# Kernel optimization log

Hardware: AMD Instinct MI355X
Metric: run time of the kernel (lower is better)

The kernel has to match this reference:

```python
import jax, jax.numpy as jnp
import numpy as np
from jax import lax

H, W, C = 24, 8, 128
HW = H * W
PART = 4
SA_K = 49  # CBAM spatial-attention kernel size (default of CBAMBlock)
EPS = 1e-5


def conv2d(x, w, b, pad_h, pad_w):
    y = lax.conv_general_dilated(x, w, (1, 1), [(pad_h, pad_h), (pad_w, pad_w)],
                                 dimension_numbers=('NCHW', 'OIHW', 'NCHW'))
    return y + b[None, :, None, None]


def cbam(x, se_w1, se_w2, sa_w, sa_b):
    # Channel attention: shared MLP on global max- and avg-pooled descriptors.
    mx = x.max(axis=(2, 3))          # [n, c]
    av = x.mean(axis=(2, 3))         # [n, c]
    def se(v):
        return jax.nn.relu(v @ se_w1.T) @ se_w2.T
    ca = jax.nn.sigmoid(se(mx) + se(av))[:, :, None, None]
    out = x * ca
    # Spatial attention: 49x49 conv on [max, mean] over channels.
    smx = out.max(axis=1, keepdims=True)
    sav = out.mean(axis=1, keepdims=True)
    s = jnp.concatenate([smx, sav], axis=1)      # [n, 2, H, W]
    sa = jax.nn.sigmoid(conv2d(s, sa_w, sa_b, SA_K // 2, SA_K // 2))
    return out * sa + x


def position_aware_max(score6, dim):
    # score6: [p, g, hr, wr, hs, ws]; fixed-length (part_rows) row window,
    # start clamped to [0, h - part_rows] -> vectorized sliding-window max.
    part_rows = H // PART
    half = part_rows // 2
    starts = jnp.clip(jnp.arange(H) - half, 0, H - part_rows)
    if dim == 0:
        m = score6.max(axis=3)            # max over wr -> [p, g, hr, hs, ws]
        mi = jnp.moveaxis(m, 3, 0)        # [hs, p, g, hr, ws]
        def f(m_i, st):
            return lax.dynamic_slice_in_dim(m_i, st, part_rows, axis=2).max(axis=2)
        out = jax.vmap(f)(mi, starts)     # [h, p, g, ws]
    else:
        m = score6.max(axis=5)            # max over ws -> [p, g, hr, wr, hs]
        mi = jnp.moveaxis(m, 2, 0)        # [hr, p, g, wr, hs]
        def f(m_i, st):
            return lax.dynamic_slice_in_dim(m_i, st, part_rows, axis=3).max(axis=3)
        out = jax.vmap(f)(mi, starts)     # [h, p, g, wr]
    p, g = score6.shape[0], score6.shape[1]
    return jnp.moveaxis(out, 0, 2).reshape(p, g, HW)


def bn_eval(x, gamma, beta, mean, var):
    return (x - mean) * (gamma / jnp.sqrt(var + EPS)) + beta


def setup_inputs() -> dict:
    key = jax.random.key(0)
    ks = jax.random.split(key, 8)
    red = 16
    return {
        'prob_fea': jax.random.normal(ks[0], (32, C, H, W), jnp.float32),
        'gal_fea': jax.random.normal(ks[1], (32, C, H, W), jnp.float32),
        'se_w1': jax.random.normal(ks[2], (C // red, C), jnp.float32) * 0.05,
        'se_w2': jax.random.normal(ks[3], (C, C // red), jnp.float32) * 0.05,
        'sa_w': jax.random.normal(ks[4], (1, 2, SA_K, SA_K), jnp.float32) * 0.02,
        'sa_b': jnp.zeros((1,), jnp.float32),
        'bn_g': jnp.ones((1,), jnp.float32),
        'bn_b': jnp.zeros((1,), jnp.float32),
        'bn_m': jnp.zeros((1,), jnp.float32),
        'bn_v': jnp.ones((1,), jnp.float32),
        'fc_w': jnp.full((1, HW), 1.0 / HW, jnp.float32),
        'fc_b': jax.random.normal(ks[5], (1,), jnp.float32) * 0.01,
        'lbn_g': jnp.ones((1,), jnp.float32),
        'lbn_b': jnp.zeros((1,), jnp.float32),
        'lbn_m': jnp.zeros((1,), jnp.float32),
        'lbn_v': jnp.ones((1,), jnp.float32),
    }


def reference(prob_fea, gal_fea, se_w1, se_w2, sa_w, sa_b,
              bn_g, bn_b, bn_m, bn_v, fc_w, fc_b,
              lbn_g, lbn_b, lbn_m, lbn_v):
    pf = cbam(prob_fea, se_w1, se_w2, sa_w, sa_b)
    gf = cbam(gal_fea, se_w1, se_w2, sa_w, sa_b)
    p, g = pf.shape[0], gf.shape[0]
    pf = pf.reshape(p, C, HW)
    gf = gf.reshape(g, C, HW)
    # pairwise feature matching: [p, g, r(gal spatial), s(prob spatial)]
    score = jnp.einsum('pcs,gcr->pgrs', pf, gf)
    score6 = score.reshape(p, g, H, W, H, W)
    s1 = position_aware_max(score6, 0)  # [p, g, HW]
    s2 = position_aware_max(score6, 1)  # [p, g, HW]
    sc = jnp.concatenate([s1, s2], axis=-1).reshape(-1, HW)  # [p*g*2, HW]
    sc = bn_eval(sc, bn_g, bn_b, bn_m, bn_v)
    y = sc @ fc_w.T + fc_b                  # [p*g*2, 1]
    y = y.reshape(-1, 2).sum(axis=1, keepdims=True)
    y = bn_eval(y, lbn_g, lbn_b, lbn_m, lbn_v)
    return jax.nn.sigmoid(y).reshape(p, g)
```

## Files before the change

kernel.cpp:

```cpp
#include <hip/hip_runtime.h>
#include <hip/hip_bf16.h>

#define HH 24
#define WW 8
#define HWSZ 192
#define CC 128
#define EPSV 1e-5f

#define M1LD 200
#define M2LD 28

typedef __attribute__((ext_vector_type(8))) short bf16x8;
typedef __attribute__((ext_vector_type(4))) float f32x4;

__device__ __forceinline__ float sigmoidf_(float x) { return 1.0f / (1.0f + expf(-x)); }

__device__ __forceinline__ unsigned short f2bf(float f) {
    unsigned int u = __float_as_uint(f);
    unsigned int r = (u + 0x7fffu + ((u >> 16) & 1u)) >> 16;
    return (unsigned short)r;
}
__device__ __forceinline__ float bf2f(unsigned short s) {
    return __uint_as_float((unsigned int)s << 16);
}

__global__ __launch_bounds__(512) void cbam_stats(
    const float* __restrict__ prob, const float* __restrict__ gal,
    const float* __restrict__ se_w1, const float* __restrict__ se_w2,
    const float* __restrict__ sa_w, const float* __restrict__ sa_b,
    float* __restrict__ ca_out, float* __restrict__ sa_out)
{
    __shared__ float mxs[CC], avs[CC], hid[16], cas[CC];
    __shared__ float smx2[2 * HWSZ], sav2[2 * HWSZ];
    __shared__ float wbuf[2 * 49 * 49];

    int n = blockIdx.x;
    const float* x = (n < 32) ? prob + (size_t)n * CC * HWSZ : gal + (size_t)(n - 32) * CC * HWSZ;

    int tid = threadIdx.x, l = tid & 63, w = tid >> 6;

    for (int i = tid; i < 2 * 49 * 49; i += 512) wbuf[i] = sa_w[i];

    for (int i = 0; i < 16; ++i) {
        int c = w * 16 + i;
        const float* row = x + c * HWSZ;
        float a = row[l], b = row[l + 64], d = row[l + 128];
        float mv = fmaxf(a, fmaxf(b, d));
        float sv = a + b + d;
        #pragma unroll
        for (int m = 1; m < 64; m <<= 1) {
            mv = fmaxf(mv, __shfl_xor(mv, m));
            sv += __shfl_xor(sv, m);
        }
        if (l == 0) { mxs[c] = mv; avs[c] = sv * (1.0f / HWSZ); }
    }
    __syncthreads();

    if (tid < 256) {
        int j = tid >> 4, chunk = tid & 15;
        const float* v = (j < 8) ? mxs : avs;
        const float* wrow = se_w1 + (j & 7) * CC + chunk * 8;
        const float* vv = v + chunk * 8;
        float acc = 0.f;
        #pragma unroll
        for (int k = 0; k < 8; ++k) acc += vv[k] * wrow[k];
        #pragma unroll
        for (int m = 1; m < 16; m <<= 1) acc += __shfl_xor(acc, m);
        if (chunk == 0) hid[j] = fmaxf(acc, 0.f);
    }
    __syncthreads();

    if (tid < CC) {
        float acc = 0.f;
        #pragma unroll
        for (int j = 0; j < 8; ++j) acc += (hid[j] + hid[8 + j]) * se_w2[tid * 8 + j];
        cas[tid] = sigmoidf_(acc);
        ca_out[n * CC + tid] = cas[tid];
    }
    __syncthreads();

    if (tid < 2 * HWSZ) {
        int s = tid >> 1, half = tid & 1;
        int c0 = half * 64;
        float mv = -INFINITY, sv = 0.f;
        #pragma unroll 4
        for (int k = 0; k < 64; ++k) {
            float v = x[(c0 + k) * HWSZ + s] * cas[c0 + k];
            mv = fmaxf(mv, v); sv += v;
        }
        smx2[half * HWSZ + s] = mv; sav2[half * HWSZ + s] = sv;
    }
    __syncthreads();

    if (tid < HWSZ) {
        int y = tid >> 3, xx = tid & 7;
        float acc = sa_b[0];
        for (int iy = 0; iy < HH; ++iy) {
            int wy = iy - y + 24;
            const float* w0 = wbuf + wy * 49;
            const float* w1 = wbuf + 2401 + wy * 49;
            #pragma unroll
            for (int ix = 0; ix < WW; ++ix) {
                int wx = ix - xx + 24;
                int sp = iy * 8 + ix;
                float s0 = fmaxf(smx2[sp], smx2[HWSZ + sp]);
                float s1 = (sav2[sp] + sav2[HWSZ + sp]) * (1.0f / CC);
                acc += s0 * w0[wx] + s1 * w1[wx];
            }
        }
        sa_out[n * HWSZ + tid] = sigmoidf_(acc);
    }
}

__global__ __launch_bounds__(256) void cbam_apply(
    const float* __restrict__ prob, const float* __restrict__ gal,
    const float* __restrict__ ca_buf, const float* __restrict__ sa_buf,
    __hip_bfloat16* __restrict__ pf_t, __hip_bfloat16* __restrict__ gf_t)
{
    __shared__ unsigned short T[16][136];
    __shared__ float sash[16];

    int n = blockIdx.x / 12;
    int s0 = (blockIdx.x % 12) * 16;
    const float* x = (n < 32) ? prob + (size_t)n * CC * HWSZ : gal + (size_t)(n - 32) * CC * HWSZ;
    __hip_bfloat16* dst = (n < 32) ? pf_t + (size_t)n * HWSZ * CC : gf_t + (size_t)(n - 32) * HWSZ * CC;

    int tid = threadIdx.x;
    if (tid < 16) sash[tid] = sa_buf[n * HWSZ + s0 + tid];
    __syncthreads();

    int c = tid >> 1, half = tid & 1;
    float ca = ca_buf[n * CC + c];
    const float* xp = x + c * HWSZ + s0 + half * 8;
    float4 va = *(const float4*)xp;
    float4 vb = *(const float4*)(xp + 4);
    int r0 = half * 8;
    T[r0 + 0][c] = f2bf(va.x * (1.f + ca * sash[r0 + 0]));
    T[r0 + 1][c] = f2bf(va.y * (1.f + ca * sash[r0 + 1]));
    T[r0 + 2][c] = f2bf(va.z * (1.f + ca * sash[r0 + 2]));
    T[r0 + 3][c] = f2bf(va.w * (1.f + ca * sash[r0 + 3]));
    T[r0 + 4][c] = f2bf(vb.x * (1.f + ca * sash[r0 + 4]));
    T[r0 + 5][c] = f2bf(vb.y * (1.f + ca * sash[r0 + 5]));
    T[r0 + 6][c] = f2bf(vb.z * (1.f + ca * sash[r0 + 6]));
    T[r0 + 7][c] = f2bf(vb.w * (1.f + ca * sash[r0 + 7]));
    __syncthreads();

    int s_l = tid >> 4, c8 = (tid & 15) * 8;
    const unsigned int* src = (const unsigned int*)&T[s_l][c8];
    unsigned int* d32 = (unsigned int*)(dst + (s0 + s_l) * CC + c8);
    d32[0] = src[0]; d32[1] = src[1]; d32[2] = src[2]; d32[3] = src[3];
}

__global__ __launch_bounds__(384) void score_kernel(
    const __hip_bfloat16* __restrict__ pf_t, const __hip_bfloat16* __restrict__ gf_t,
    const float* __restrict__ bn_g, const float* __restrict__ bn_b,
    const float* __restrict__ bn_m, const float* __restrict__ bn_v,
    const float* __restrict__ fc_w, const float* __restrict__ fc_b,
    const float* __restrict__ lbn_g, const float* __restrict__ lbn_b,
    const float* __restrict__ lbn_m, const float* __restrict__ lbn_v,
    float* __restrict__ out)
{
    __shared__ __align__(16) char bstage[2][4096];
    __shared__ unsigned short M1b[24 * M1LD];
    __shared__ unsigned short M2b[HWSZ * M2LD];
    __shared__ float red[6], wred[6];

    int bi = blockIdx.x;
    int p = bi >> 5, g = bi & 31;
    int tid = threadIdx.x, l = tid & 63, w = tid >> 6;

    const __hip_bfloat16* A = gf_t + (size_t)g * HWSZ * CC;
    const __hip_bfloat16* B = pf_t + (size_t)p * HWSZ * CC;

    int row_a = l & 15;
    int koff = (l >> 4) * 8;

    #define STAGE_B(bufidx, st_)                                                         \
        if (w < 4) {                                                                     \
            const __hip_bfloat16* src = B + ((st_) * 16 + (l & 15)) * CC                 \
                                          + (w * 4 + (l >> 4)) * 8;                      \
            __builtin_amdgcn_global_load_lds(                                            \
                (const __attribute__((address_space(1))) void*)src,                      \
                (__attribute__((address_space(3))) void*)(&bstage[bufidx][w * 1024]),    \
                16, 0, 0);                                                               \
        }

    STAGE_B(0, 0)

    bf16x8 afr[2][4];
    #pragma unroll
    for (int rt = 0; rt < 2; ++rt) {
        const __hip_bfloat16* ap = A + (w * 32 + rt * 16 + row_a) * CC + koff;
        #pragma unroll
        for (int ks = 0; ks < 4; ++ks)
            afr[rt][ks] = *(const bf16x8*)(ap + ks * 32);
    }
    __syncthreads();

    for (int st = 0; st < 12; ++st) {
        int cur = st & 1;
        if (st < 11) { STAGE_B(cur ^ 1, st + 1) }

        const char* bb = bstage[cur];
        bf16x8 b0 = *(const bf16x8*)(bb + 0 * 1024 + l * 16);
        bf16x8 b1 = *(const bf16x8*)(bb + 1 * 1024 + l * 16);
        bf16x8 b2 = *(const bf16x8*)(bb + 2 * 1024 + l * 16);
        bf16x8 b3 = *(const bf16x8*)(bb + 3 * 1024 + l * 16);

        #pragma unroll
        for (int rt = 0; rt < 2; ++rt) {
            f32x4 acc = {0.f, 0.f, 0.f, 0.f};
            acc = __builtin_amdgcn_mfma_f32_16x16x32_bf16(afr[rt][0], b0, acc, 0, 0, 0);
            acc = __builtin_amdgcn_mfma_f32_16x16x32_bf16(afr[rt][1], b1, acc, 0, 0, 0);
            acc = __builtin_amdgcn_mfma_f32_16x16x32_bf16(afr[rt][2], b2, acc, 0, 0, 0);
            acc = __builtin_amdgcn_mfma_f32_16x16x32_bf16(afr[rt][3], b3, acc, 0, 0, 0);

            int RT = w * 2 + rt;

            float mrow = fmaxf(fmaxf(acc[0], acc[1]), fmaxf(acc[2], acc[3]));
            mrow = fmaxf(mrow, __shfl_xor(mrow, 16));
            if (((l >> 4) & 1) == 0)
                M1b[(2 * RT + (l >> 5)) * M1LD + st * 16 + (l & 15)] = f2bf(mrow);

            float v0 = acc[0], v1 = acc[1], v2 = acc[2], v3 = acc[3];
            #pragma unroll
            for (int m = 1; m < 8; m <<= 1) {
                v0 = fmaxf(v0, __shfl_xor(v0, m));
                v1 = fmaxf(v1, __shfl_xor(v1, m));
                v2 = fmaxf(v2, __shfl_xor(v2, m));
                v3 = fmaxf(v3, __shfl_xor(v3, m));
            }
            if ((l & 7) == 0) {
                int hs = st * 2 + ((l >> 3) & 1);
                int rbase = RT * 16 + (l >> 4) * 4;
                M2b[(rbase + 0) * M2LD + hs] = f2bf(v0);
                M2b[(rbase + 1) * M2LD + hs] = f2bf(v1);
                M2b[(rbase + 2) * M2LD + hs] = f2bf(v2);
                M2b[(rbase + 3) * M2LD + hs] = f2bf(v3);
            }
        }
        __syncthreads();
    }

    float part = 0.f, wpart = 0.f;
    if (tid < HWSZ) {
        int h = tid >> 3;
        int st0 = h - 3; if (st0 < 0) st0 = 0; if (st0 > 18) st0 = 18;
        float v1 = -INFINITY, v2 = -INFINITY;
        #pragma unroll
        for (int i = 0; i < 6; ++i) {
            v1 = fmaxf(v1, bf2f(M1b[(st0 + i) * M1LD + tid]));
            v2 = fmaxf(v2, bf2f(M2b[tid * M2LD + st0 + i]));
        }
        float fw = fc_w[tid];
        part = fw * (v1 + v2);
        wpart = fw;
    }
    #pragma unroll
    for (int m = 1; m < 64; m <<= 1) {
        part  += __shfl_xor(part, m);
        wpart += __shfl_xor(wpart, m);
    }
    if (l == 0) { red[w] = part; wred[w] = wpart; }
    __syncthreads();

    if (tid == 0) {
        float total = red[0] + red[1] + red[2] + red[3] + red[4] + red[5];
        float Wsum  = wred[0] + wred[1] + wred[2] + wred[3] + wred[4] + wred[5];
        float k1 = bn_g[0] * rsqrtf(bn_v[0] + EPSV);
        float Y = k1 * total + 2.f * ((bn_b[0] - k1 * bn_m[0]) * Wsum + fc_b[0]);
        float kl = lbn_g[0] * rsqrtf(lbn_v[0] + EPSV);
        float Z = (Y - lbn_m[0]) * kl + lbn_b[0];
        out[bi] = 1.f / (1.f + expf(-Z));
    }
}

extern "C" void kernel_launch(void* const* d_in, const int* in_sizes, int n_in,
                              void* d_out, int out_size, void* d_ws, size_t ws_size,
                              hipStream_t stream)
{
    const float* prob  = (const float*)d_in[0];
    const float* gal   = (const float*)d_in[1];
    const float* se_w1 = (const float*)d_in[2];
    const float* se_w2 = (const float*)d_in[3];
    const float* sa_w  = (const float*)d_in[4];
    const float* sa_b  = (const float*)d_in[5];
    const float* bn_g  = (const float*)d_in[6];
    const float* bn_b  = (const float*)d_in[7];
    const float* bn_m  = (const float*)d_in[8];
    const float* bn_v  = (const float*)d_in[9];
    const float* fc_w  = (const float*)d_in[10];
    const float* fc_b  = (const float*)d_in[11];
    const float* lbn_g = (const float*)d_in[12];
    const float* lbn_b = (const float*)d_in[13];
    const float* lbn_m = (const float*)d_in[14];
    const float* lbn_v = (const float*)d_in[15];

    __hip_bfloat16* pf_t = (__hip_bfloat16*)d_ws;
    __hip_bfloat16* gf_t = pf_t + (size_t)32 * HWSZ * CC;
    float* ca_buf = (float*)(gf_t + (size_t)32 * HWSZ * CC);
    float* sa_buf = ca_buf + 64 * CC;
    float* out = (float*)d_out;

    cbam_stats<<<64, 512, 0, stream>>>(prob, gal, se_w1, se_w2, sa_w, sa_b, ca_buf, sa_buf);
    cbam_apply<<<768, 256, 0, stream>>>(prob, gal, ca_buf, sa_buf, pf_t, gf_t);
    score_kernel<<<1024, 384, 0, stream>>>(pf_t, gf_t, bn_g, bn_b, bn_m, bn_v,
                                           fc_w, fc_b, lbn_g, lbn_b, lbn_m, lbn_v, out);
}
```

Measured before the change: 154.0 us.

## Preload all B tiles to LDS and compute transposed MFMA for column max

Loads the whole 192x128 probe tile into LDS up front instead of double-buffering one stage at a time, which removes the per-stage barrier inside the score loop. It also issues a second, operand-swapped MFMA chain so the column-direction max can be taken with a single xor-shuffle instead of a three-step shuffle butterfly over four values. This doubles MFMA work and raises LDS use to about 48KB per block for staging alone, which may lower occupancy.

```diff
diff --git a/kernel.cpp b/kernel.cpp
--- a/kernel.cpp
+++ b/kernel.cpp
@@ -160,7 +160,7 @@
     const float* __restrict__ lbn_m, const float* __restrict__ lbn_v,
     float* __restrict__ out)
 {
-    __shared__ __align__(16) char bstage[2][4096];
+    __shared__ __align__(16) char Bs[12 * 4096];
     __shared__ unsigned short M1b[24 * M1LD];
     __shared__ unsigned short M2b[HWSZ * M2LD];
     __shared__ float red[6], wred[6];
@@ -172,21 +172,19 @@
     const __hip_bfloat16* A = gf_t + (size_t)g * HWSZ * CC;
     const __hip_bfloat16* B = pf_t + (size_t)p * HWSZ * CC;
 
+    #pragma unroll
+    for (int i = 0; i < 8; ++i) {
+        int idx = w * 8 + i;
+        const __hip_bfloat16* src = B + ((idx >> 2) * 16 + (l & 15)) * CC
+                                      + ((idx & 3) * 4 + (l >> 4)) * 8;
+        __builtin_amdgcn_global_load_lds(
+            (const __attribute__((address_space(1))) void*)src,
+            (__attribute__((address_space(3))) void*)(&Bs[idx * 1024]),
+            16, 0, 0);
+    }
+
     int row_a = l & 15;
     int koff = (l >> 4) * 8;
-
-    #define STAGE_B(bufidx, st_)                                                         \
-        if (w < 4) {                                                                     \
-            const __hip_bfloat16* src = B + ((st_) * 16 + (l & 15)) * CC                 \
-                                          + (w * 4 + (l >> 4)) * 8;                      \
-            __builtin_amdgcn_global_load_lds(                                            \
-                (const __attribute__((address_space(1))) void*)src,                      \
-                (__attribute__((address_space(3))) void*)(&bstage[bufidx][w * 1024]),    \
-                16, 0, 0);                                                               \
-        }
-
-    STAGE_B(0, 0)
-
     bf16x8 afr[2][4];
     #pragma unroll
     for (int rt = 0; rt < 2; ++rt) {
@@ -198,10 +196,7 @@
     __syncthreads();
 
     for (int st = 0; st < 12; ++st) {
-        int cur = st & 1;
-        if (st < 11) { STAGE_B(cur ^ 1, st + 1) }
-
-        const char* bb = bstage[cur];
+        const char* bb = Bs + st * 4096;
         bf16x8 b0 = *(const bf16x8*)(bb + 0 * 1024 + l * 16);
         bf16x8 b1 = *(const bf16x8*)(bb + 1 * 1024 + l * 16);
         bf16x8 b2 = *(const bf16x8*)(bb + 2 * 1024 + l * 16);
@@ -209,38 +204,31 @@
 
         #pragma unroll
         for (int rt = 0; rt < 2; ++rt) {
-            f32x4 acc = {0.f, 0.f, 0.f, 0.f};
-            acc = __builtin_amdgcn_mfma_f32_16x16x32_bf16(afr[rt][0], b0, acc, 0, 0, 0);
-            acc = __builtin_amdgcn_mfma_f32_16x16x32_bf16(afr[rt][1], b1, acc, 0, 0, 0);
-            acc = __builtin_amdgcn_mfma_f32_16x16x32_bf16(afr[rt][2], b2, acc, 0, 0, 0);
-            acc = __builtin_amdgcn_mfma_f32_16x16x32_bf16(afr[rt][3], b3, acc, 0, 0, 0);
+            f32x4 acc1 = {0.f, 0.f, 0.f, 0.f};
+            f32x4 acc2 = {0.f, 0.f, 0.f, 0.f};
+            acc1 = __builtin_amdgcn_mfma_f32_16x16x32_bf16(afr[rt][0], b0, acc1, 0, 0, 0);
+            acc2 = __builtin_amdgcn_mfma_f32_16x16x32_bf16(b0, afr[rt][0], acc2, 0, 0, 0);
+            acc1 = __builtin_amdgcn_mfma_f32_16x16x32_bf16(afr[rt][1], b1, acc1, 0, 0, 0);
+            acc2 = __builtin_amdgcn_mfma_f32_16x16x32_bf16(b1, afr[rt][1], acc2, 0, 0, 0);
+            acc1 = __builtin_amdgcn_mfma_f32_16x16x32_bf16(afr[rt][2], b2, acc1, 0, 0, 0);
+            acc2 = __builtin_amdgcn_mfma_f32_16x16x32_bf16(b2, afr[rt][2], acc2, 0, 0, 0);
+            acc1 = __builtin_amdgcn_mfma_f32_16x16x32_bf16(afr[rt][3], b3, acc1, 0, 0, 0);
+            acc2 = __builtin_amdgcn_mfma_f32_16x16x32_bf16(b3, afr[rt][3], acc2, 0, 0, 0);
 
             int RT = w * 2 + rt;
 
-            float mrow = fmaxf(fmaxf(acc[0], acc[1]), fmaxf(acc[2], acc[3]));
+            float mrow = fmaxf(fmaxf(acc1[0], acc1[1]), fmaxf(acc1[2], acc1[3]));
             mrow = fmaxf(mrow, __shfl_xor(mrow, 16));
             if (((l >> 4) & 1) == 0)
                 M1b[(2 * RT + (l >> 5)) * M1LD + st * 16 + (l & 15)] = f2bf(mrow);
 
-            float v0 = acc[0], v1 = acc[1], v2 = acc[2], v3 = acc[3];
-            #pragma unroll
-            for (int m = 1; m < 8; m <<= 1) {
-                v0 = fmaxf(v0, __shfl_xor(v0, m));
-                v1 = fmaxf(v1, __shfl_xor(v1, m));
-                v2 = fmaxf(v2, __shfl_xor(v2, m));
-                v3 = fmaxf(v3, __shfl_xor(v3, m));
-            }
-            if ((l & 7) == 0) {
-                int hs = st * 2 + ((l >> 3) & 1);
-                int rbase = RT * 16 + (l >> 4) * 4;
-                M2b[(rbase + 0) * M2LD + hs] = f2bf(v0);
-                M2b[(rbase + 1) * M2LD + hs] = f2bf(v1);
-                M2b[(rbase + 2) * M2LD + hs] = f2bf(v2);
-                M2b[(rbase + 3) * M2LD + hs] = f2bf(v3);
-            }
-        }
-        __syncthreads();
-    }
+            float mcol = fmaxf(fmaxf(acc2[0], acc2[1]), fmaxf(acc2[2], acc2[3]));
+            mcol = fmaxf(mcol, __shfl_xor(mcol, 16));
+            if (((l >> 4) & 1) == 0)
+                M2b[(RT * 16 + (l & 15)) * M2LD + st * 2 + (l >> 5)] = f2bf(mcol);
+        }
+    }
+    __syncthreads();
 
     float part = 0.f, wpart = 0.f;
     if (tid < HWSZ) {
```

Result: no change. 151.8 us (-1.4%).
